# Kernel optimization log

Measured on AMD Instinct MI355X. Metric: run time of the kernel, lower is better.

Reference implementation:

```python
import jax, jax.numpy as jnp
import numpy as np

N_BINS = 15  # init kwarg n_bins


def setup_inputs() -> dict:
    key = jax.random.key(0)
    k1, k2, k3, k4 = jax.random.split(key, 4)
    B, T = 8192, 4096
    confidences = jax.random.uniform(k1, (B, T), dtype=jnp.float32)
    predictions = jax.random.randint(k2, (B, T), 0, 3, dtype=jnp.int32)
    targets = jax.random.randint(k3, (B, T), 0, 3, dtype=jnp.int32)
    mask = jax.random.randint(k4, (B, T), 0, 2, dtype=jnp.int32)
    return {"confidences": confidences, "predictions": predictions,
            "targets": targets, "mask": mask}


def reference(confidences, predictions, targets, mask):
    # Flatten, as in the torch forward.
    c = confidences.reshape(-1)
    p = predictions.reshape(-1)
    t = targets.reshape(-1)
    w = mask.reshape(-1).astype(c.dtype)  # 1.0 where valid, 0.0 where masked out

    n = N_BINS
    # Bin b covers (b/n, (b+1)/n]: for c in (0,1], bin index = ceil(c*n) - 1.
    idx = jnp.clip(jnp.ceil(c * n).astype(jnp.int32) - 1, 0, n - 1)
    # c == 0 falls in no bin (strict lower bound on first bin), c > 1 in none.
    in_range = ((c > 0.0) & (c <= 1.0)).astype(c.dtype)
    wv = w * in_range  # effective per-element weight for bin statistics

    counts = jax.ops.segment_sum(wv, idx, num_segments=n)              # n_b
    conf_sum = jax.ops.segment_sum(wv * c, idx, num_segments=n)        # sum conf per bin
    corr = (p == t).astype(c.dtype)
    corr_sum = jax.ops.segment_sum(wv * corr, idx, num_segments=n)     # sum correct per bin

    total = jnp.sum(w)  # len(confidences) after masking
    safe = jnp.maximum(counts, jnp.asarray(1.0, c.dtype))
    avg_conf = conf_sum / safe
    acc = corr_sum / safe
    ece = jnp.sum(jnp.where(counts > 0, jnp.abs(avg_conf - acc) * counts / total, 0.0))
    return ece
```

## Files before the change

kernel.cpp:

```cpp
#include <hip/hip_runtime.h>

#define NBINS 15

typedef float f32x4 __attribute__((ext_vector_type(4)));
typedef int   i32x4 __attribute__((ext_vector_type(4)));


#define PROC(cv, pv, tv, mv)                                              \
    {                                                                     \
        _Pragma("unroll")                                                 \
        for (int k = 0; k < 4; ++k) {                                     \
            float c = (cv)[k];                                            \
            int   m = (mv)[k];                                            \
            tot += (unsigned int)m;                                       \
            bool valid = (m != 0) & (c > 0.0f) & (c <= 1.0f);             \
            int bin = (int)ceilf(c * 15.0f) - 1;                          \
            bin = min(max(bin, 0), NBINS - 1);                            \
            bin = valid ? bin : -1;                                       \
            float corr = ((pv)[k] == (tv)[k]) ? 1.0f : 0.0f;              \
            int d = (int)rintf((c - corr) * 65536.0f);                    \
            _Pragma("unroll")                                             \
            for (int b = 0; b < NBINS; ++b)                               \
                acc[b] += (bin == b) ? d : 0;                             \
        }                                                                 \
    }

__global__ __launch_bounds__(256, 6) void ece_partial(
    const float* __restrict__ conf,
    const int*   __restrict__ pred,
    const int*   __restrict__ targ,
    const int*   __restrict__ mask,
    unsigned long long* __restrict__ ws,
    int nvec)
{
    __shared__ unsigned int hsum[16];
    __shared__ unsigned long long stot;

    const int tid  = threadIdx.x;
    const int lane = tid & 63;

    if (tid < 16) hsum[tid] = 0u;
    if (tid == 0) stot = 0ULL;
    __syncthreads();

    const int gid    = blockIdx.x * blockDim.x + tid;
    const int stride = gridDim.x * blockDim.x;

    const f32x4* __restrict__ c4p = (const f32x4*)conf;
    const i32x4* __restrict__ p4p = (const i32x4*)pred;
    const i32x4* __restrict__ t4p = (const i32x4*)targ;
    const i32x4* __restrict__ m4p = (const i32x4*)mask;

    int acc[NBINS];
#pragma unroll
    for (int b = 0; b < NBINS; ++b) acc[b] = 0;

    unsigned int tot = 0;

    int k = gid;
    if (k + stride < nvec) {
        f32x4 c0 = __builtin_nontemporal_load(c4p + k);
        i32x4 p0 = __builtin_nontemporal_load(p4p + k);
        i32x4 t0 = __builtin_nontemporal_load(t4p + k);
        i32x4 m0 = __builtin_nontemporal_load(m4p + k);
        f32x4 c1 = __builtin_nontemporal_load(c4p + (k + stride));
        i32x4 p1 = __builtin_nontemporal_load(p4p + (k + stride));
        i32x4 t1 = __builtin_nontemporal_load(t4p + (k + stride));
        i32x4 m1 = __builtin_nontemporal_load(m4p + (k + stride));

        for (; k + 3 * stride < nvec; k += 2 * stride) {
            PROC(c0, p0, t0, m0);
            {
                const int n0 = k + 2 * stride;
                c0 = __builtin_nontemporal_load(c4p + n0);
                p0 = __builtin_nontemporal_load(p4p + n0);
                t0 = __builtin_nontemporal_load(t4p + n0);
                m0 = __builtin_nontemporal_load(m4p + n0);
            }
            PROC(c1, p1, t1, m1);
            {
                const int n1 = k + 3 * stride;
                c1 = __builtin_nontemporal_load(c4p + n1);
                p1 = __builtin_nontemporal_load(p4p + n1);
                t1 = __builtin_nontemporal_load(t4p + n1);
                m1 = __builtin_nontemporal_load(m4p + n1);
            }
        }
        PROC(c0, p0, t0, m0);
        PROC(c1, p1, t1, m1);
        k += 2 * stride;
    }
    for (; k < nvec; k += stride) {
        f32x4 cz = __builtin_nontemporal_load(c4p + k);
        i32x4 pz = __builtin_nontemporal_load(p4p + k);
        i32x4 tz = __builtin_nontemporal_load(t4p + k);
        i32x4 mz = __builtin_nontemporal_load(m4p + k);
        PROC(cz, pz, tz, mz);
    }

#pragma unroll
    for (int b = 0; b < NBINS; ++b) {
        int v = acc[b];
#pragma unroll
        for (int off = 32; off; off >>= 1) v += __shfl_down(v, off, 64);
        acc[b] = v;
    }
    unsigned int v = tot;
#pragma unroll
    for (int off = 32; off; off >>= 1) v += __shfl_down(v, off, 64);

    if (lane == 0) {
#pragma unroll
        for (int b = 0; b < NBINS; ++b)
            if (acc[b] != 0) atomicAdd(&hsum[b], (unsigned int)acc[b]);
        atomicAdd(&stot, (unsigned long long)v);
    }
    __syncthreads();

    if (tid < NBINS) {
        int s = (int)hsum[tid];
        if (s != 0)
            atomicAdd(&ws[tid], (unsigned long long)(long long)s);
    }
    if (tid == 0) {
        unsigned long long s = stot;
        if (s) atomicAdd(&ws[NBINS], s);
    }
}

__global__ void ece_scalar_tail(const float* __restrict__ conf,
                                const int*   __restrict__ pred,
                                const int*   __restrict__ targ,
                                const int*   __restrict__ mask,
                                unsigned long long* __restrict__ ws,
                                long long start, long long n)
{
    long long i = start + threadIdx.x;
    if (i < n) {
        float c = conf[i];
        int   m = mask[i];
        if (m) atomicAdd(&ws[NBINS], 1ULL);
        if ((m != 0) & (c > 0.0f) & (c <= 1.0f)) {
            int bin = (int)ceilf(c * 15.0f) - 1;
            bin = min(max(bin, 0), NBINS - 1);
            float corr = (pred[i] == targ[i]) ? 1.0f : 0.0f;
            int d = (int)rintf((c - corr) * 65536.0f);
            atomicAdd(&ws[bin], (unsigned long long)(long long)d);
        }
    }
}

__global__ void ece_final(const unsigned long long* __restrict__ ws,
                          float* __restrict__ out)
{
    int tid = threadIdx.x;
    double v = 0.0;
    if (tid < NBINS) {
        long long s = (long long)ws[tid];
        v = fabs((double)s);
    }
#pragma unroll
    for (int off = 32; off; off >>= 1) v += __shfl_down(v, off, 64);
    if (tid == 0) {
        double total = (double)ws[NBINS];
        if (total < 1.0) total = 1.0;
        out[0] = (float)(v * (1.0 / 65536.0) / total);
    }
}

extern "C" void kernel_launch(void* const* d_in, const int* in_sizes, int n_in,
                              void* d_out, int out_size, void* d_ws, size_t ws_size,
                              hipStream_t stream)
{
    const float* conf = (const float*)d_in[0];
    const int*   pred = (const int*)d_in[1];
    const int*   targ = (const int*)d_in[2];
    const int*   mask = (const int*)d_in[3];
    long long n    = in_sizes[0];
    int       nvec = (int)(n / 4);

    unsigned long long* ws = (unsigned long long*)d_ws;

    hipMemsetAsync(d_ws, 0, (NBINS + 1) * sizeof(unsigned long long), stream);

    ece_partial<<<1536, 256, 0, stream>>>(conf, pred, targ, mask, ws, nvec);
    if (n % 4 != 0) {
        ece_scalar_tail<<<1, 64, 0, stream>>>(conf, pred, targ, mask, ws,
                                              (long long)nvec * 4, n);
    }
    ece_final<<<1, 64, 0, stream>>>(ws, (float*)d_out);
}
```

Measured before the change: 112.1 us.

## Fuse final reduction into partial kernel via last-block ticket and deepen prefetch

Merges the partial-sum, scalar-tail and final kernels into a single launch. A global ticket counter lets the last block to finish read the bin totals and write the ECE result, which removes one kernel launch and its dependency gap. The tail elements are now handled by block 0 inside the main kernel. The load pipeline also goes from double to triple buffering, so more loads are in flight at the cost of extra registers, which may pressure occupancy at the 6-waves launch bound.

```diff
diff --git a/kernel.cpp b/kernel.cpp
--- a/kernel.cpp
+++ b/kernel.cpp
@@ -25,22 +25,33 @@
         }                                                                 \
     }
 
-__global__ __launch_bounds__(256, 6) void ece_partial(
+#define LOADSTAGE(cv, pv, tv, mv, idx)                                    \
+    {                                                                     \
+        const int _i = (idx);                                             \
+        cv = __builtin_nontemporal_load(c4p + _i);                        \
+        pv = __builtin_nontemporal_load(p4p + _i);                        \
+        tv = __builtin_nontemporal_load(t4p + _i);                        \
+        mv = __builtin_nontemporal_load(m4p + _i);                        \
+    }
+
+__global__ __launch_bounds__(256, 6) void ece_fused(
     const float* __restrict__ conf,
     const int*   __restrict__ pred,
     const int*   __restrict__ targ,
     const int*   __restrict__ mask,
     unsigned long long* __restrict__ ws,
-    int nvec)
+    float* __restrict__ out,
+    int nvec, long long n, int nblocks)
 {
     __shared__ unsigned int hsum[16];
     __shared__ unsigned long long stot;
+    __shared__ int islast;
 
     const int tid  = threadIdx.x;
     const int lane = tid & 63;
 
     if (tid < 16) hsum[tid] = 0u;
-    if (tid == 0) stot = 0ULL;
+    if (tid == 0) { stot = 0ULL; islast = 0; }
     __syncthreads();
 
     const int gid    = blockIdx.x * blockDim.x + tid;
@@ -57,44 +68,48 @@
 
     unsigned int tot = 0;
 
+    if (blockIdx.x == 0) {
+        long long base = (long long)nvec * 4;
+        if (tid < (int)(n - base)) {
+            long long idx = base + tid;
+            float c = conf[idx];
+            int   m = mask[idx];
+            tot += (unsigned int)m;
+            bool valid = (m != 0) & (c > 0.0f) & (c <= 1.0f);
+            int bin = (int)ceilf(c * 15.0f) - 1;
+            bin = min(max(bin, 0), NBINS - 1);
+            bin = valid ? bin : -1;
+            float corr = (pred[idx] == targ[idx]) ? 1.0f : 0.0f;
+            int d = (int)rintf((c - corr) * 65536.0f);
+#pragma unroll
+            for (int b = 0; b < NBINS; ++b)
+                acc[b] += (bin == b) ? d : 0;
+        }
+    }
+
     int k = gid;
-    if (k + stride < nvec) {
-        f32x4 c0 = __builtin_nontemporal_load(c4p + k);
-        i32x4 p0 = __builtin_nontemporal_load(p4p + k);
-        i32x4 t0 = __builtin_nontemporal_load(t4p + k);
-        i32x4 m0 = __builtin_nontemporal_load(m4p + k);
-        f32x4 c1 = __builtin_nontemporal_load(c4p + (k + stride));
-        i32x4 p1 = __builtin_nontemporal_load(p4p + (k + stride));
-        i32x4 t1 = __builtin_nontemporal_load(t4p + (k + stride));
-        i32x4 m1 = __builtin_nontemporal_load(m4p + (k + stride));
+    if (k + 2 * stride < nvec) {
+        f32x4 c0, c1, c2; i32x4 p0, p1, p2, t0, t1, t2, m0, m1, m2;
+        LOADSTAGE(c0, p0, t0, m0, k);
+        LOADSTAGE(c1, p1, t1, m1, k + stride);
+        LOADSTAGE(c2, p2, t2, m2, k + 2 * stride);
 
-        for (; k + 3 * stride < nvec; k += 2 * stride) {
+        for (; k + 5 * stride < nvec; k += 3 * stride) {
             PROC(c0, p0, t0, m0);
-            {
-                const int n0 = k + 2 * stride;
-                c0 = __builtin_nontemporal_load(c4p + n0);
-                p0 = __builtin_nontemporal_load(p4p + n0);
-                t0 = __builtin_nontemporal_load(t4p + n0);
-                m0 = __builtin_nontemporal_load(m4p + n0);
-            }
+            LOADSTAGE(c0, p0, t0, m0, k + 3 * stride);
             PROC(c1, p1, t1, m1);
-            {
-                const int n1 = k + 3 * stride;
-                c1 = __builtin_nontemporal_load(c4p + n1);
-                p1 = __builtin_nontemporal_load(p4p + n1);
-                t1 = __builtin_nontemporal_load(t4p + n1);
-                m1 = __builtin_nontemporal_load(m4p + n1);
-            }
+            LOADSTAGE(c1, p1, t1, m1, k + 4 * stride);
+            PROC(c2, p2, t2, m2);
+            LOADSTAGE(c2, p2, t2, m2, k + 5 * stride);
         }
         PROC(c0, p0, t0, m0);
         PROC(c1, p1, t1, m1);
-        k += 2 * stride;
+        PROC(c2, p2, t2, m2);
+        k += 3 * stride;
     }
     for (; k < nvec; k += stride) {
-        f32x4 cz = __builtin_nontemporal_load(c4p + k);
-        i32x4 pz = __builtin_nontemporal_load(p4p + k);
-        i32x4 tz = __builtin_nontemporal_load(t4p + k);
-        i32x4 mz = __builtin_nontemporal_load(m4p + k);
+        f32x4 cz; i32x4 pz, tz, mz;
+        LOADSTAGE(cz, pz, tz, mz, k);
         PROC(cz, pz, tz, mz);
     }
 
@@ -122,49 +137,35 @@
         if (s != 0)
             atomicAdd(&ws[tid], (unsigned long long)(long long)s);
     }
+    if (tid == NBINS) {
+        atomicAdd(&ws[NBINS], stot);
+    }
+    __threadfence();
+    __syncthreads();
+
     if (tid == 0) {
-        unsigned long long s = stot;
-        if (s) atomicAdd(&ws[NBINS], s);
+        unsigned int* done = (unsigned int*)&ws[16];
+        unsigned int ticket = atomicAdd(done, 1u);
+        islast = (ticket == (unsigned int)(nblocks - 1)) ? 1 : 0;
     }
-}
+    __syncthreads();
 
-__global__ void ece_scalar_tail(const float* __restrict__ conf,
-                                const int*   __restrict__ pred,
-                                const int*   __restrict__ targ,
-                                const int*   __restrict__ mask,
-                                unsigned long long* __restrict__ ws,
-                                long long start, long long n)
-{
-    long long i = start + threadIdx.x;
-    if (i < n) {
-        float c = conf[i];
-        int   m = mask[i];
-        if (m) atomicAdd(&ws[NBINS], 1ULL);
-        if ((m != 0) & (c > 0.0f) & (c <= 1.0f)) {
-            int bin = (int)ceilf(c * 15.0f) - 1;
-            bin = min(max(bin, 0), NBINS - 1);
-            float corr = (pred[i] == targ[i]) ? 1.0f : 0.0f;
-            int d = (int)rintf((c - corr) * 65536.0f);
-            atomicAdd(&ws[bin], (unsigned long long)(long long)d);
+    if (islast && tid < 64) {
+        double dv = 0.0;
+        unsigned long long totv = 0ULL;
+        if (tid < NBINS) {
+            long long s = (long long)atomicAdd(&ws[tid], 0ULL);
+            dv = fabs((double)s);
         }
-    }
-}
-
-__global__ void ece_final(const unsigned long long* __restrict__ ws,
-                          float* __restrict__ out)
-{
-    int tid = threadIdx.x;
-    double v = 0.0;
-    if (tid < NBINS) {
-        long long s = (long long)ws[tid];
-        v = fabs((double)s);
-    }
+        if (tid == NBINS) totv = atomicAdd(&ws[NBINS], 0ULL);
 #pragma unroll
-    for (int off = 32; off; off >>= 1) v += __shfl_down(v, off, 64);
-    if (tid == 0) {
-        double total = (double)ws[NBINS];
-        if (total < 1.0) total = 1.0;
-        out[0] = (float)(v * (1.0 / 65536.0) / total);
+        for (int off = 32; off; off >>= 1) dv += __shfl_down(dv, off, 64);
+        totv = __shfl(totv, NBINS, 64);
+        if (tid == 0) {
+            double total = (double)totv;
+            if (total < 1.0) total = 1.0;
+            out[0] = (float)(dv * (1.0 / 65536.0) / total);
+        }
     }
 }
 
@@ -181,12 +182,9 @@
 
     unsigned long long* ws = (unsigned long long*)d_ws;
 
-    hipMemsetAsync(d_ws, 0, (NBINS + 1) * sizeof(unsigned long long), stream);
+    hipMemsetAsync(d_ws, 0, 17 * sizeof(unsigned long long), stream);
 
-    ece_partial<<<1536, 256, 0, stream>>>(conf, pred, targ, mask, ws, nvec);
-    if (n % 4 != 0) {
-        ece_scalar_tail<<<1, 64, 0, stream>>>(conf, pred, targ, mask, ws,
-                                              (long long)nvec * 4, n);
-    }
-    ece_final<<<1, 64, 0, stream>>>(ws, (float*)d_out);
+    const int nblocks = 1536;
+    ece_fused<<<nblocks, 256, 0, stream>>>(conf, pred, targ, mask, ws,
+                                           (float*)d_out, nvec, n, nblocks);
 }
```

Result: slower. 369.3 us (+229.6%).
